# Kernel optimization log

Measured on AMD Instinct MI355X. Metric: run time of the kernel, lower is better.

Reference implementation:

```python
import jax, jax.numpy as jnp
import numpy as np
from jax.scipy.special import logsumexp

B, T, D = 32, 448, 768
H = 256  # per-direction LSTM hidden (lstm_hidden=512, bidirectional)
NTAGS = 2


def setup_inputs() -> dict:
    key = jax.random.key(0)
    ks = jax.random.split(key, 18)
    rn = lambda i, shp, sc=1.0: jax.random.normal(ks[i], shp, jnp.float32) * sc
    w = 0.05  # small init to keep LSTM gates in a sane range
    inp = {
        'top_hidden': rn(0, (B, T, D)),
        's_feats': rn(1, (3, B, T, D)),
        't_feats': rn(2, (3, B, T, D)),
        'W_ih_f': rn(3, (4 * H, D), w), 'W_hh_f': rn(4, (4 * H, H), w),
        'b_ih_f': jnp.zeros((4 * H,), jnp.float32), 'b_hh_f': jnp.zeros((4 * H,), jnp.float32),
        'W_ih_b': rn(5, (4 * H, D), w), 'W_hh_b': rn(6, (4 * H, H), w),
        'b_ih_b': jnp.zeros((4 * H,), jnp.float32), 'b_hh_b': jnp.zeros((4 * H,), jnp.float32),
        'W_cls': rn(7, (NTAGS, 2 * H), w), 'b_cls': jnp.zeros((NTAGS,), jnp.float32),
        'crf_start': rn(8, (NTAGS,), 0.1), 'crf_end': rn(9, (NTAGS,), 0.1),
        'crf_trans': rn(10, (NTAGS, NTAGS), 0.1),
        'labels': jax.random.randint(ks[11], (B, T), 0, 2, jnp.int32),
        'mask': jnp.ones((B, T), jnp.int32),
    }
    return inp


def _lstm_dir(x, Wih, Whh, bih, bhh, reverse):
    # x: [B,T,D] -> hs: [B,T,H]; torch gate order i,f,g,o
    gx = jnp.einsum('btd,gd->btg', x, Wih) + bih + bhh  # [B,T,4H]
    def cell(carry, g_t):
        h, c = carry
        g = g_t + h @ Whh.T
        i, f, gg, o = jnp.split(g, 4, axis=-1)
        c = jax.nn.sigmoid(f) * c + jax.nn.sigmoid(i) * jnp.tanh(gg)
        h = jax.nn.sigmoid(o) * jnp.tanh(c)
        return (h, c), h
    z = jnp.zeros((x.shape[0], Whh.shape[1]), x.dtype)
    _, hs = jax.lax.scan(cell, (z, z), jnp.swapaxes(gx, 0, 1), reverse=reverse)
    return jnp.swapaxes(hs, 0, 1)


def _crf_nll(emissions, tags, m):
    # pytorch-crf log-likelihood, reduction='mean'; emissions [B,T,2], m bool [B,T] (m[:,0]=True)
    b = jnp.arange(emissions.shape[0])
    mf = m.astype(emissions.dtype)
    # numerator: score of gold path
    def _num(crf_start, crf_end, crf_trans):
        score = crf_start[tags[:, 0]] + emissions[b, 0, tags[:, 0]]
        trans_sc = crf_trans[tags[:, :-1], tags[:, 1:]]
        em_sc = jnp.take_along_axis(emissions[:, 1:, :], tags[:, 1:, None], axis=2)[..., 0]
        score = score + jnp.sum((trans_sc + em_sc) * mf[:, 1:], axis=1)
        last = tags[b, jnp.sum(m, axis=1).astype(jnp.int32) - 1]
        return score + crf_end[last]
    return _num


def reference(top_hidden, s_feats, t_feats, W_ih_f, W_hh_f, b_ih_f, b_hh_f,
              W_ih_b, W_hh_b, b_ih_b, b_hh_b, W_cls, b_cls,
              crf_start, crf_end, crf_trans, labels, mask):
    # dropout is identity here (deterministic reference / eval mode)
    h_f = _lstm_dir(top_hidden, W_ih_f, W_hh_f, b_ih_f, b_hh_f, reverse=False)
    h_b = _lstm_dir(top_hidden, W_ih_b, W_hh_b, b_ih_b, b_hh_b, reverse=True)
    h = jnp.concatenate([h_f, h_b], axis=-1)           # [B,T,512]
    logits = h @ W_cls.T + b_cls                        # [B,T,2]

    m = mask.astype(bool).at[:, 0].set(True)
    tags = jnp.where(labels == -100, 0, labels)

    numerator = _crf_nll(logits, tags, m)(crf_start, crf_end, crf_trans)  # [B]

    # partition function via forward algorithm (lax.scan over time)
    alpha = crf_start[None, :] + logits[:, 0]           # [B,2]
    def step(alpha, inp):
        em_t, m_t = inp                                  # [B,2], [B]
        nxt = logsumexp(alpha[:, :, None] + crf_trans[None] + em_t[:, None, :], axis=1)
        return jnp.where(m_t[:, None], nxt, alpha), None
    alpha, _ = jax.lax.scan(step, alpha,
                            (jnp.swapaxes(logits[:, 1:], 0, 1), jnp.swapaxes(m[:, 1:], 0, 1)))
    logZ = logsumexp(alpha + crf_end[None, :], axis=1)  # [B]

    span_loss = -jnp.mean(numerator - logZ)

    # KD: mean of per-layer MSE (equal-size layers => overall mean); teacher is no-grad
    kd_loss = jnp.mean((s_feats - jax.lax.stop_gradient(t_feats)) ** 2)

    loss = 0.5 * span_loss + 0.5 * kd_loss
    return loss
```

## Files before the change

kernel.cpp:

```cpp
#include <hip/hip_runtime.h>
#include <hip/hip_bf16.h>

typedef unsigned int uint;
typedef unsigned short ushort;
typedef __attribute__((ext_vector_type(8))) short short8;
typedef __attribute__((ext_vector_type(4))) float floatx4;

#define BB 32
#define TT 448
#define DD 768
#define HH 256
#define G4 1024
#define BT 14336
#define NBX 4
#define NWV 16

constexpr size_t OFF_XB   = 0;
constexpr size_t OFF_WIH  = 22020096;
constexpr size_t OFF_WHH  = OFF_WIH + 3145728;
constexpr size_t OFF_BIAS = OFF_WHH + 1048576;
constexpr size_t OFF_GX   = OFF_BIAS + 8192;
constexpr size_t OFF_HB   = OFF_GX + 58720256;
constexpr size_t OFF_LP   = OFF_HB + 14712832;
constexpr size_t OFF_CNT  = OFF_LP + 114688;
constexpr size_t OFF_KD   = OFF_CNT + 4096;

__device__ __forceinline__ ushort f2bf(float x) {
    uint u = __float_as_uint(x);
    uint r = (u + 0x7FFFu + ((u >> 16) & 1u)) >> 16;
    return (ushort)r;
}
__device__ __forceinline__ float bf2f(ushort s) {
    return __uint_as_float(((uint)s) << 16);
}
__device__ __forceinline__ float fsig(float x) {
    return __builtin_amdgcn_rcpf(1.0f + __expf(-x));
}
__device__ __forceinline__ float ftanh(float x) {
    return 2.0f * __builtin_amdgcn_rcpf(1.0f + __expf(-2.0f * x)) - 1.0f;
}
__device__ __forceinline__ float lse2(float x, float y) {
    float m = fmaxf(x, y);
    return m + logf(expf(x - m) + expf(y - m));
}

__device__ __forceinline__ void st_sc1_b64(void* addr, uint2 v) {
    asm volatile("global_store_dwordx2 %0, %1, off sc0 sc1" :: "v"(addr), "v"(v) : "memory");
}
__device__ __forceinline__ int ld_flag_sc1(const int* addr) {
    int r;
    asm volatile("global_load_dword %0, %1, off sc0 sc1\n\t"
                 "s_waitcnt vmcnt(0)"
                 : "=&v"(r) : "v"(addr) : "memory");
    return r;
}
#define WAIT_VM0() asm volatile("s_waitcnt vmcnt(0)" ::: "memory")

__global__ __launch_bounds__(256) void prep_kernel(
    const float* __restrict__ x,
    const float* __restrict__ wif, const float* __restrict__ wib,
    const float* __restrict__ whf, const float* __restrict__ whb,
    const float* __restrict__ bif, const float* __restrict__ bhf,
    const float* __restrict__ bib, const float* __restrict__ bhb,
    ushort* __restrict__ xb, ushort* __restrict__ wihb,
    ushort* __restrict__ whhb, float* __restrict__ bias,
    float* __restrict__ lp, int* __restrict__ cnt,
    float* __restrict__ kd_sum)
{
    size_t i0 = (size_t)blockIdx.x * 256 + threadIdx.x;
    if (i0 == 0) kd_sum[0] = 0.f;
    const size_t NX = (size_t)BT * DD;
    const size_t NW = (size_t)G4 * DD;
    const size_t NH = (size_t)G4 * HH;
    const size_t B0 = NX + 2 * NW + 2 * NH;
    const size_t B1 = B0 + 2048;
    const size_t B2 = B1 + 28672;
    const size_t TOT = B2 + 1024;
    const size_t stride = (size_t)gridDim.x * 256;
    for (size_t idx = i0; idx < TOT; idx += stride) {
        if (idx < NX) {
            xb[idx] = f2bf(x[idx]);
        } else if (idx < NX + 2 * NW) {
            size_t j = idx - NX;
            wihb[j] = f2bf(j < NW ? wif[j] : wib[j - NW]);
        } else if (idx < NX + 2 * NW + 2 * NH) {
            size_t j = idx - NX - 2 * NW;
            whhb[j] = f2bf(j < NH ? whf[j] : whb[j - NH]);
        } else if (idx < B1) {
            size_t j = idx - B0;
            bias[j] = (j < 1024) ? (bif[j] + bhf[j]) : (bib[j - 1024] + bhb[j - 1024]);
        } else if (idx < B2) {
            lp[idx - B1] = 0.f;
        } else {
            cnt[idx - B2] = 0;
        }
    }
}

__global__ __launch_bounds__(256) void kd_kernel(
    const float4* __restrict__ s, const float4* __restrict__ t,
    float* __restrict__ kd_sum, int n4)
{
    __shared__ float sred[4];
    float acc = 0.f;
    size_t stride = (size_t)gridDim.x * 256;
    for (size_t i = (size_t)blockIdx.x * 256 + threadIdx.x; i < (size_t)n4; i += stride) {
        float4 a = s[i], b = t[i];
        float d0 = a.x - b.x, d1 = a.y - b.y, d2 = a.z - b.z, d3 = a.w - b.w;
        acc += d0 * d0 + d1 * d1 + d2 * d2 + d3 * d3;
    }
    for (int off = 32; off; off >>= 1) acc += __shfl_down(acc, off, 64);
    int lane = threadIdx.x & 63, wv = threadIdx.x >> 6;
    if (lane == 0) sred[wv] = acc;
    __syncthreads();
    if (threadIdx.x == 0) atomicAdd(kd_sum, sred[0] + sred[1] + sred[2] + sred[3]);
}

__global__ __launch_bounds__(256) void gemm_gx(
    const ushort* __restrict__ xb, const ushort* __restrict__ wih,
    const float* __restrict__ bias, ushort* __restrict__ gx)
{
    int dir = blockIdx.z;
    const ushort* W = wih + (size_t)dir * G4 * DD;
    ushort* out = gx + (size_t)dir * BT * G4;
    int tid = threadIdx.x;
    int wave = tid >> 6, lane = tid & 63;
    int quad = lane >> 4, r16 = lane & 15;
    int m0 = blockIdx.x * 64 + wave * 16;
    int n0 = blockIdx.y * 64;
    floatx4 acc[4];
    #pragma unroll
    for (int i = 0; i < 4; i++) acc[i] = (floatx4){0.f, 0.f, 0.f, 0.f};

    const ushort* aptr = xb + (size_t)(m0 + r16) * DD + quad * 8;
    const ushort* bptr = W + (size_t)(n0 + r16) * DD + quad * 8;
    for (int k = 0; k < DD; k += 32) {
        short8 af = *(const short8*)(aptr + k);
        #pragma unroll
        for (int nt = 0; nt < 4; nt++) {
            short8 bf = *(const short8*)(bptr + (size_t)nt * 16 * DD + k);
            acc[nt] = __builtin_amdgcn_mfma_f32_16x16x32_bf16(af, bf, acc[nt], 0, 0, 0);
        }
    }
    #pragma unroll
    for (int nt = 0; nt < 4; nt++) {
        int col = n0 + nt * 16 + r16;
        float bv = bias[dir * G4 + col];
        #pragma unroll
        for (int i = 0; i < 4; i++) {
            int row = m0 + quad * 4 + i;
            int b = row / TT, t = row % TT;
            out[((size_t)t * BB + b) * G4 + col] = f2bf(acc[nt][i] + bv);
        }
    }
}

__global__ __launch_bounds__(256, 1) void lstm_rec(
    const ushort* __restrict__ gxall,
    const ushort* __restrict__ whhb,
    const float* __restrict__ Wcls,
    ushort* __restrict__ hbuf,
    int* __restrict__ cnt,
    float* __restrict__ lp)
{
    int bx = blockIdx.x;
    int dir = blockIdx.y;
    int tid = threadIdx.x;
    int w = tid >> 6, lane = tid & 63;
    int quad = lane >> 4, r16 = lane & 15;
    int dbase = bx * 64 + w * 16;

    short8 wfrag[4][8];
    const ushort* wsrc = whhb + (size_t)dir * (G4 * HH);
    #pragma unroll
    for (int g = 0; g < 4; g++)
        #pragma unroll
        for (int kt = 0; kt < 8; kt++)
            wfrag[g][kt] = *(const short8*)(wsrc + (size_t)(g * 256 + dbase + r16) * HH + kt * 32 + quad * 8);

    float wc0[4], wc1[4];
    #pragma unroll
    for (int r = 0; r < 4; r++) {
        int d = dbase + quad * 4 + r;
        wc0[r] = Wcls[dir * 256 + d];
        wc1[r] = Wcls[512 + dir * 256 + d];
    }
    float cst[2][4];
    #pragma unroll
    for (int mt = 0; mt < 2; mt++)
        #pragma unroll
        for (int r = 0; r < 4; r++) cst[mt][r] = 0.f;

    const ushort* gxd = gxall + (size_t)dir * BT * G4;
    ushort* hb = hbuf + (size_t)dir * 449 * BB * HH;
    int* cn = cnt + dir * 449;

    for (int s = 0; s < TT; s++) {
        int t = dir ? (TT - 1 - s) : s;
        uint2 gxv[4][2];
        #pragma unroll
        for (int g = 0; g < 4; g++)
            #pragma unroll
            for (int mt = 0; mt < 2; mt++)
                gxv[g][mt] = *(const uint2*)(gxd + ((size_t)t * BB + mt * 16 + r16) * G4
                                             + g * 256 + dbase + quad * 4);

        floatx4 acc[4][2];
        #pragma unroll
        for (int g = 0; g < 4; g++)
            #pragma unroll
            for (int mt = 0; mt < 2; mt++)
                acc[g][mt] = (floatx4){
                    bf2f((ushort)(gxv[g][mt].x & 0xFFFFu)),
                    bf2f((ushort)(gxv[g][mt].x >> 16)),
                    bf2f((ushort)(gxv[g][mt].y & 0xFFFFu)),
                    bf2f((ushort)(gxv[g][mt].y >> 16))};

        if (s > 0) {
            while (ld_flag_sc1(&cn[s]) < NWV) {}
            const ushort* hsrc = hb + (size_t)s * (BB * HH);
            const ushort* h0 = hsrc + (size_t)r16 * HH + quad * 8;
            const ushort* h1 = hsrc + (size_t)(16 + r16) * HH + quad * 8;
            int4 hA0, hA1, hA2, hA3, hA4, hA5, hA6, hA7;
            int4 hB0, hB1, hB2, hB3, hB4, hB5, hB6, hB7;
            asm volatile(
                "global_load_dwordx4 %0, %16, off sc0 sc1\n\t"
                "global_load_dwordx4 %1, %16, off offset:64 sc0 sc1\n\t"
                "global_load_dwordx4 %2, %16, off offset:128 sc0 sc1\n\t"
                "global_load_dwordx4 %3, %16, off offset:192 sc0 sc1\n\t"
                "global_load_dwordx4 %4, %16, off offset:256 sc0 sc1\n\t"
                "global_load_dwordx4 %5, %16, off offset:320 sc0 sc1\n\t"
                "global_load_dwordx4 %6, %16, off offset:384 sc0 sc1\n\t"
                "global_load_dwordx4 %7, %16, off offset:448 sc0 sc1\n\t"
                "global_load_dwordx4 %8, %17, off sc0 sc1\n\t"
                "global_load_dwordx4 %9, %17, off offset:64 sc0 sc1\n\t"
                "global_load_dwordx4 %10, %17, off offset:128 sc0 sc1\n\t"
                "global_load_dwordx4 %11, %17, off offset:192 sc0 sc1\n\t"
                "global_load_dwordx4 %12, %17, off offset:256 sc0 sc1\n\t"
                "global_load_dwordx4 %13, %17, off offset:320 sc0 sc1\n\t"
                "global_load_dwordx4 %14, %17, off offset:384 sc0 sc1\n\t"
                "global_load_dwordx4 %15, %17, off offset:448 sc0 sc1\n\t"
                "s_waitcnt vmcnt(0)"
                : "=&v"(hA0), "=&v"(hA1), "=&v"(hA2), "=&v"(hA3),
                  "=&v"(hA4), "=&v"(hA5), "=&v"(hA6), "=&v"(hA7),
                  "=&v"(hB0), "=&v"(hB1), "=&v"(hB2), "=&v"(hB3),
                  "=&v"(hB4), "=&v"(hB5), "=&v"(hB6), "=&v"(hB7)
                : "v"(h0), "v"(h1)
                : "memory");
            short8 hf[2][8];
            hf[0][0] = *(short8*)&hA0; hf[0][1] = *(short8*)&hA1;
            hf[0][2] = *(short8*)&hA2; hf[0][3] = *(short8*)&hA3;
            hf[0][4] = *(short8*)&hA4; hf[0][5] = *(short8*)&hA5;
            hf[0][6] = *(short8*)&hA6; hf[0][7] = *(short8*)&hA7;
            hf[1][0] = *(short8*)&hB0; hf[1][1] = *(short8*)&hB1;
            hf[1][2] = *(short8*)&hB2; hf[1][3] = *(short8*)&hB3;
            hf[1][4] = *(short8*)&hB4; hf[1][5] = *(short8*)&hB5;
            hf[1][6] = *(short8*)&hB6; hf[1][7] = *(short8*)&hB7;
            #pragma unroll
            for (int kt = 0; kt < 8; kt++)
                #pragma unroll
                for (int g = 0; g < 4; g++)
                    #pragma unroll
                    for (int mt = 0; mt < 2; mt++)
                        acc[g][mt] = __builtin_amdgcn_mfma_f32_16x16x32_bf16(
                            wfrag[g][kt], hf[mt][kt], acc[g][mt], 0, 0, 0);
        }

        ushort* hdst = hb + (size_t)(s + 1) * (BB * HH);
        float lv0[2], lv1[2];
        #pragma unroll
        for (int mt = 0; mt < 2; mt++) {
            float l0 = 0.f, l1 = 0.f;
            uint pk[2];
            #pragma unroll
            for (int r = 0; r < 4; r++) {
                float ig = fsig(acc[0][mt][r]);
                float fg = fsig(acc[1][mt][r]);
                float gg = ftanh(acc[2][mt][r]);
                float og = fsig(acc[3][mt][r]);
                float c = fg * cst[mt][r] + ig * gg;
                cst[mt][r] = c;
                float h = og * ftanh(c);
                uint hb16 = (uint)f2bf(h);
                if (r & 1) pk[r >> 1] |= hb16 << 16; else pk[r >> 1] = hb16;
                l0 += h * wc0[r];
                l1 += h * wc1[r];
            }
            st_sc1_b64(hdst + (size_t)(mt * 16 + r16) * HH + dbase + quad * 4,
                       make_uint2(pk[0], pk[1]));
            lv0[mt] = l0; lv1[mt] = l1;
        }
        WAIT_VM0();
        __hip_atomic_fetch_add(&cn[s + 1], 1, __ATOMIC_RELAXED, __HIP_MEMORY_SCOPE_AGENT);

        #pragma unroll
        for (int mt = 0; mt < 2; mt++) {
            lv0[mt] += __shfl_xor(lv0[mt], 16, 64);
            lv0[mt] += __shfl_xor(lv0[mt], 32, 64);
            lv1[mt] += __shfl_xor(lv1[mt], 16, 64);
            lv1[mt] += __shfl_xor(lv1[mt], 32, 64);
        }
        if (quad == 0) {
            #pragma unroll
            for (int mt = 0; mt < 2; mt++) {
                int b = mt * 16 + r16;
                atomicAdd(&lp[((size_t)t * BB + b) * 2 + 0], lv0[mt]);
                atomicAdd(&lp[((size_t)t * BB + b) * 2 + 1], lv1[mt]);
            }
        }
    }
}

__global__ void crf_loss(
    const float* __restrict__ lp, const float* __restrict__ bcls,
    const float* __restrict__ cs, const float* __restrict__ ce,
    const float* __restrict__ ct, const int* __restrict__ labels,
    const int* __restrict__ mask, const float* __restrict__ kd_sum,
    float* __restrict__ out)
{
    int b = threadIdx.x;
    float val = 0.f;
    if (b < BB) {
        float bc0 = bcls[0], bc1 = bcls[1];
        float T00 = ct[0], T01 = ct[1], T10 = ct[2], T11 = ct[3];
        const int* lab = labels + (size_t)b * TT;
        const int* mk = mask + (size_t)b * TT;

        float e0 = lp[(size_t)b * 2 + 0] + bc0;
        float e1 = lp[(size_t)b * 2 + 1] + bc1;
        int y0 = lab[0];
        y0 = (y0 == -100) ? 0 : y0;
        float num = cs[y0] + (y0 ? e1 : e0);
        float a0 = cs[0] + e0, a1 = cs[1] + e1;
        int prev = y0;
        int msum = 1;
        for (int t = 1; t < TT; t++) {
            e0 = lp[((size_t)t * BB + b) * 2 + 0] + bc0;
            e1 = lp[((size_t)t * BB + b) * 2 + 1] + bc1;
            int y = lab[t];
            y = (y == -100) ? 0 : y;
            int mt = (mk[t] != 0);
            float mf = mt ? 1.f : 0.f;
            float trans = ct[prev * 2 + y];
            float em = y ? e1 : e0;
            num += (trans + em) * mf;
            float n0 = lse2(a0 + T00, a1 + T10) + e0;
            float n1 = lse2(a0 + T01, a1 + T11) + e1;
            if (mt) { a0 = n0; a1 = n1; }
            prev = y;
            msum += mt;
        }
        int last = lab[msum - 1];
        last = (last == -100) ? 0 : last;
        num += ce[last];
        float logZ = lse2(a0 + ce[0], a1 + ce[1]);
        val = num - logZ;
    }
    for (int off = 32; off; off >>= 1) val += __shfl_down(val, off, 64);
    if (threadIdx.x == 0) {
        float span = -(val / (float)BB);
        float kd = kd_sum[0] / (float)(3u * BB * TT * DD);
        out[0] = 0.5f * span + 0.5f * kd;
    }
}

extern "C" void kernel_launch(void* const* d_in, const int* in_sizes, int n_in,
                              void* d_out, int out_size, void* d_ws, size_t ws_size,
                              hipStream_t stream) {
    const float* x    = (const float*)d_in[0];
    const float* sf   = (const float*)d_in[1];
    const float* tfp  = (const float*)d_in[2];
    const float* wif  = (const float*)d_in[3];
    const float* whf  = (const float*)d_in[4];
    const float* bif  = (const float*)d_in[5];
    const float* bhf  = (const float*)d_in[6];
    const float* wib  = (const float*)d_in[7];
    const float* whb  = (const float*)d_in[8];
    const float* bib  = (const float*)d_in[9];
    const float* bhb  = (const float*)d_in[10];
    const float* wcls = (const float*)d_in[11];
    const float* bcls = (const float*)d_in[12];
    const float* cs   = (const float*)d_in[13];
    const float* ce   = (const float*)d_in[14];
    const float* ct   = (const float*)d_in[15];
    const int* labels = (const int*)d_in[16];
    const int* mask   = (const int*)d_in[17];
    float* out = (float*)d_out;

    char* ws = (char*)d_ws;
    ushort* xb   = (ushort*)(ws + OFF_XB);
    ushort* wihb = (ushort*)(ws + OFF_WIH);
    ushort* whhb = (ushort*)(ws + OFF_WHH);
    float* bias  = (float*)(ws + OFF_BIAS);
    ushort* gx   = (ushort*)(ws + OFF_GX);
    ushort* hbuf = (ushort*)(ws + OFF_HB);
    float* lp    = (float*)(ws + OFF_LP);
    int* cnt     = (int*)(ws + OFF_CNT);
    float* kd    = (float*)(ws + OFF_KD);

    prep_kernel<<<1024, 256, 0, stream>>>(x, wif, wib, whf, whb, bif, bhf, bib, bhb,
                                          xb, wihb, whhb, bias, lp, cnt, kd);
    kd_kernel<<<2048, 256, 0, stream>>>((const float4*)sf, (const float4*)tfp, kd,
                                        (int)(3u * BB * TT * DD / 4u));
    gemm_gx<<<dim3(224, 16, 2), 256, 0, stream>>>(xb, wihb, bias, gx);
    lstm_rec<<<dim3(NBX, 2), 256, 0, stream>>>(gx, whhb, wcls, hbuf, cnt, lp);
    crf_loss<<<1, 64, 0, stream>>>(lp, bcls, cs, ce, ct, labels, mask, kd, out);
}
```

Before: 2.993 ms.

## Replace atomic step counters with per-wave flags and atomic-free logit partials

The recurrent LSTM kernel now signals step completion by having each wave store its own flag word, and waiters poll all 16 flags in parallel with a ballot, instead of an atomic counter increment per wave that is spun on. The per-timestep classifier logit atomicAdds are replaced by plain stores into a per-wave partial buffer, which a new small kernel sums before the CRF. This aims to cut atomic latency and contention on the serial critical path of the recurrence. In exchange it adds an extra kernel launch and more workspace memory.

```diff
diff --git a/kernel.cpp b/kernel.cpp
--- a/kernel.cpp
+++ b/kernel.cpp
@@ -17,13 +17,14 @@
 
 constexpr size_t OFF_XB   = 0;
 constexpr size_t OFF_WIH  = 22020096;
-constexpr size_t OFF_WHH  = OFF_WIH + 3145728;
-constexpr size_t OFF_BIAS = OFF_WHH + 1048576;
-constexpr size_t OFF_GX   = OFF_BIAS + 8192;
-constexpr size_t OFF_HB   = OFF_GX + 58720256;
-constexpr size_t OFF_LP   = OFF_HB + 14712832;
-constexpr size_t OFF_CNT  = OFF_LP + 114688;
-constexpr size_t OFF_KD   = OFF_CNT + 4096;
+constexpr size_t OFF_WHH  = 25165824;
+constexpr size_t OFF_BIAS = 26214400;
+constexpr size_t OFF_GX   = 26222592;
+constexpr size_t OFF_HB   = 84942848;
+constexpr size_t OFF_SEQ  = 99655680;
+constexpr size_t OFF_LPP  = 99721216;
+constexpr size_t OFF_LP   = 107061248;
+constexpr size_t OFF_KD   = 107175936;
 
 __device__ __forceinline__ ushort f2bf(float x) {
     uint u = __float_as_uint(x);
@@ -47,7 +48,10 @@
 __device__ __forceinline__ void st_sc1_b64(void* addr, uint2 v) {
     asm volatile("global_store_dwordx2 %0, %1, off sc0 sc1" :: "v"(addr), "v"(v) : "memory");
 }
-__device__ __forceinline__ int ld_flag_sc1(const int* addr) {
+__device__ __forceinline__ void st_sc1_b32(void* addr, int v) {
+    asm volatile("global_store_dword %0, %1, off sc0 sc1" :: "v"(addr), "v"(v) : "memory");
+}
+__device__ __forceinline__ int ld_sc1_b32(const int* addr) {
     int r;
     asm volatile("global_load_dword %0, %1, off sc0 sc1\n\t"
                  "s_waitcnt vmcnt(0)"
@@ -64,8 +68,7 @@
     const float* __restrict__ bib, const float* __restrict__ bhb,
     ushort* __restrict__ xb, ushort* __restrict__ wihb,
     ushort* __restrict__ whhb, float* __restrict__ bias,
-    float* __restrict__ lp, int* __restrict__ cnt,
-    float* __restrict__ kd_sum)
+    int* __restrict__ seq, float* __restrict__ kd_sum)
 {
     size_t i0 = (size_t)blockIdx.x * 256 + threadIdx.x;
     if (i0 == 0) kd_sum[0] = 0.f;
@@ -74,8 +77,7 @@
     const size_t NH = (size_t)G4 * HH;
     const size_t B0 = NX + 2 * NW + 2 * NH;
     const size_t B1 = B0 + 2048;
-    const size_t B2 = B1 + 28672;
-    const size_t TOT = B2 + 1024;
+    const size_t TOT = B1 + 2 * 449 * 16;
     const size_t stride = (size_t)gridDim.x * 256;
     for (size_t idx = i0; idx < TOT; idx += stride) {
         if (idx < NX) {
@@ -89,10 +91,8 @@
         } else if (idx < B1) {
             size_t j = idx - B0;
             bias[j] = (j < 1024) ? (bif[j] + bhf[j]) : (bib[j - 1024] + bhb[j - 1024]);
-        } else if (idx < B2) {
-            lp[idx - B1] = 0.f;
         } else {
-            cnt[idx - B2] = 0;
+            seq[idx - B1] = 0;
         }
     }
 }
@@ -160,8 +160,8 @@
     const ushort* __restrict__ whhb,
     const float* __restrict__ Wcls,
     ushort* __restrict__ hbuf,
-    int* __restrict__ cnt,
-    float* __restrict__ lp)
+    int* __restrict__ seq,
+    float* __restrict__ lp_part)
 {
     int bx = blockIdx.x;
     int dir = blockIdx.y;
@@ -169,6 +169,7 @@
     int w = tid >> 6, lane = tid & 63;
     int quad = lane >> 4, r16 = lane & 15;
     int dbase = bx * 64 + w * 16;
+    int slot = dir * 16 + bx * 4 + w;
 
     short8 wfrag[4][8];
     const ushort* wsrc = whhb + (size_t)dir * (G4 * HH);
@@ -193,7 +194,7 @@
 
     const ushort* gxd = gxall + (size_t)dir * BT * G4;
     ushort* hb = hbuf + (size_t)dir * 449 * BB * HH;
-    int* cn = cnt + dir * 449;
+    int* sq = seq + dir * 449 * 16;
 
     for (int s = 0; s < TT; s++) {
         int t = dir ? (TT - 1 - s) : s;
@@ -217,7 +218,11 @@
                     bf2f((ushort)(gxv[g][mt].y >> 16))};
 
         if (s > 0) {
-            while (ld_flag_sc1(&cn[s]) < NWV) {}
+            const int* pa = sq + s * 16 + (lane & 15);
+            for (;;) {
+                int v = ld_sc1_b32(pa);
+                if (__ballot(v != 0) == ~0ull) break;
+            }
             const ushort* hsrc = hb + (size_t)s * (BB * HH);
             const ushort* h0 = hsrc + (size_t)r16 * HH + quad * 8;
             const ushort* h1 = hsrc + (size_t)(16 + r16) * HH + quad * 8;
@@ -291,7 +296,7 @@
             lv0[mt] = l0; lv1[mt] = l1;
         }
         WAIT_VM0();
-        __hip_atomic_fetch_add(&cn[s + 1], 1, __ATOMIC_RELAXED, __HIP_MEMORY_SCOPE_AGENT);
+        if (lane == 0) st_sc1_b32(sq + (s + 1) * 16 + bx * 4 + w, 1);
 
         #pragma unroll
         for (int mt = 0; mt < 2; mt++) {
@@ -304,11 +309,23 @@
             #pragma unroll
             for (int mt = 0; mt < 2; mt++) {
                 int b = mt * 16 + r16;
-                atomicAdd(&lp[((size_t)t * BB + b) * 2 + 0], lv0[mt]);
-                atomicAdd(&lp[((size_t)t * BB + b) * 2 + 1], lv1[mt]);
+                *(float2*)(lp_part + ((size_t)(t * 32 + slot) * 32 + b) * 2) =
+                    make_float2(lv0[mt], lv1[mt]);
             }
         }
     }
+}
+
+__global__ __launch_bounds__(64) void lp_sum(
+    const float* __restrict__ lp_part, float* __restrict__ lp)
+{
+    int t = blockIdx.x;
+    int tid = threadIdx.x;
+    const float* p = lp_part + (size_t)t * 2048 + tid;
+    float s = 0.f;
+    #pragma unroll
+    for (int k = 0; k < 32; k++) s += p[k * 64];
+    lp[(size_t)t * 64 + tid] = s;
 }
 
 __global__ void crf_loss(
@@ -388,21 +405,23 @@
     float* out = (float*)d_out;
 
     char* ws = (char*)d_ws;
-    ushort* xb   = (ushort*)(ws + OFF_XB);
-    ushort* wihb = (ushort*)(ws + OFF_WIH);
-    ushort* whhb = (ushort*)(ws + OFF_WHH);
-    float* bias  = (float*)(ws + OFF_BIAS);
-    ushort* gx   = (ushort*)(ws + OFF_GX);
-    ushort* hbuf = (ushort*)(ws + OFF_HB);
-    float* lp    = (float*)(ws + OFF_LP);
-    int* cnt     = (int*)(ws + OFF_CNT);
-    float* kd    = (float*)(ws + OFF_KD);
+    ushort* xb    = (ushort*)(ws + OFF_XB);
+    ushort* wihb  = (ushort*)(ws + OFF_WIH);
+    ushort* whhb  = (ushort*)(ws + OFF_WHH);
+    float* bias   = (float*)(ws + OFF_BIAS);
+    ushort* gx    = (ushort*)(ws + OFF_GX);
+    ushort* hbuf  = (ushort*)(ws + OFF_HB);
+    int* seq      = (int*)(ws + OFF_SEQ);
+    float* lppart = (float*)(ws + OFF_LPP);
+    float* lp     = (float*)(ws + OFF_LP);
+    float* kd     = (float*)(ws + OFF_KD);
 
     prep_kernel<<<1024, 256, 0, stream>>>(x, wif, wib, whf, whb, bif, bhf, bib, bhb,
-                                          xb, wihb, whhb, bias, lp, cnt, kd);
+                                          xb, wihb, whhb, bias, seq, kd);
     kd_kernel<<<2048, 256, 0, stream>>>((const float4*)sf, (const float4*)tfp, kd,
                                         (int)(3u * BB * TT * DD / 4u));
     gemm_gx<<<dim3(224, 16, 2), 256, 0, stream>>>(xb, wihb, bias, gx);
-    lstm_rec<<<dim3(NBX, 2), 256, 0, stream>>>(gx, whhb, wcls, hbuf, cnt, lp);
+    lstm_rec<<<dim3(NBX, 2), 256, 0, stream>>>(gx, whhb, wcls, hbuf, seq, lppart);
+    lp_sum<<<448, 64, 0, stream>>>(lppart, lp);
     crf_loss<<<1, 64, 0, stream>>>(lp, bcls, cs, ce, ct, labels, mask, kd, out);
 }
```

After: 2.888 ms. 1.04x faster.
